# Optimization experiments

Measured on AMD Instinct MI355X. Metric: run time of the kernel, lower is better.

The kernel has to match this reference:

```python
import jax, jax.numpy as jnp
import numpy as np

N = 50000      # nodes
E = 800000     # edges
F = 32         # num_features (per-irrep channels, L=1 -> scalar + vector parts)
NINV = 128     # num_inv_features
NL = 4         # num_layers
H = 64         # edge-MLP hidden width (mlp_params)
G = 2048       # number of graphs
EPS = 1e-6


def setup_inputs() -> dict:
    key = jax.random.key(0)
    ks = jax.random.split(key, 24)
    inp = {
        "x": jax.random.normal(ks[0], (N, 5), jnp.float32),
        "pos": jax.random.normal(ks[1], (N, 3), jnp.float32),
        "edge_index": jax.random.randint(ks[2], (2, E), 0, N, jnp.int64),
        "edge_attr": jax.random.uniform(ks[3], (E, 4), jnp.float32),
        "batch": jnp.sort(jax.random.randint(ks[4], (N,), 0, G, jnp.int64)),
        # embedding block params (scalar and vector branches)
        "W_es": jax.random.normal(ks[5], (5, F), jnp.float32) * 0.3,
        "b_es": jnp.zeros((F,), jnp.float32),
        "W_ev": jax.random.normal(ks[6], (5, F), jnp.float32) * 0.3,
        # per-layer message-passing params, stacked over layers
        "W1": jax.random.normal(ks[7], (NL, 5, H), jnp.float32) * 0.3,
        "b1": jnp.zeros((NL, H), jnp.float32),
        "W2": jax.random.normal(ks[8], (NL, H, 3 * F), jnp.float32) * 0.1,
        "b2": jnp.zeros((NL, 3 * F), jnp.float32),
        "Ws": jax.random.normal(ks[9], (NL, F, F), jnp.float32) * 0.1,
        "Wv": jax.random.normal(ks[10], (NL, F, F), jnp.float32) * 0.1,
        # invariant map
        "W_inv": jax.random.normal(ks[11], (2 * F, NINV), jnp.float32) * 0.1,
        "b_inv": jnp.zeros((NINV,), jnp.float32),
        # fc head: BN -> ELU -> Linear -> BN -> ELU -> Linear(->1)
        "g1": jnp.ones((NINV,), jnp.float32),
        "be1": jnp.zeros((NINV,), jnp.float32),
        "Wf1": jax.random.normal(ks[12], (NINV, NINV), jnp.float32) * 0.1,
        "bf1": jnp.zeros((NINV,), jnp.float32),
        "g2": jnp.ones((NINV,), jnp.float32),
        "be2": jnp.zeros((NINV,), jnp.float32),
        "Wf2": jax.random.normal(ks[13], (NINV, 1), jnp.float32) * 0.1,
        "bf2": jnp.zeros((1,), jnp.float32),
    }
    return inp


def _bn(z, g, b):
    m = z.mean(0)
    va = z.var(0)
    return (z - m) * jax.lax.rsqrt(va + 1e-5) * g + b


def reference(x, pos, edge_index, edge_attr, batch,
              W_es, b_es, W_ev, W1, b1, W2, b2, Ws, Wv,
              W_inv, b_inv, g1, be1, Wf1, bf1, g2, be2, Wf2, bf2):
    src, dst = edge_index[0], edge_index[1]
    delta = pos[dst] - pos[src]                       # [E,3]
    d = jnp.sqrt(jnp.sum(delta * delta, -1) + EPS)    # [E]
    u = delta / d[:, None]                            # unit edge direction

    # embedding: L=1 steerable features = scalar [N,F] + vector [N,F,3]
    s = x @ W_es + b_es
    v = (x @ W_ev)[:, :, None] * pos[:, None, :]

    edge_in = jnp.concatenate([d[:, None], edge_attr], -1)   # [E,5]
    counts = jax.ops.segment_sum(jnp.ones((E,), s.dtype), dst, num_segments=N)
    denom = jnp.maximum(counts, 1.0)[:, None]

    for l in range(NL):  # residual message-passing blocks
        h = jax.nn.elu(edge_in @ W1[l] + b1[l]) @ W2[l] + b2[l]  # [E,3F]
        gs, gv, gsv = jnp.split(h, 3, axis=-1)
        ms = gs * s[src]                                          # [E,F]
        mv = gv[:, :, None] * v[src] + (gsv * s[src])[:, :, None] * u[:, None, :]  # [E,F,3]
        as_ = jax.ops.segment_sum(ms, dst, num_segments=N) / denom
        av = jax.ops.segment_sum(mv, dst, num_segments=N) / denom[:, :, None]
        s = s + jax.nn.elu(as_ @ Ws[l])
        v = v + jnp.einsum('nfd,fg->ngd', av, Wv[l])

    # invariant map: scalars + vector norms
    inv_feats = jnp.concatenate([s, jnp.sqrt(jnp.sum(v * v, -1) + EPS)], -1)
    inv = inv_feats @ W_inv + b_inv                               # [N,NINV]

    # global mean pool over graphs
    gcnt = jnp.maximum(jax.ops.segment_sum(jnp.ones((N,), inv.dtype), batch, num_segments=G), 1.0)[:, None]
    xg = jax.ops.segment_sum(inv, batch, num_segments=G) / gcnt   # [G,NINV]

    z = jax.nn.elu(_bn(xg, g1, be1)) @ Wf1 + bf1
    z = jax.nn.elu(_bn(z, g2, be2)) @ Wf2 + bf2                   # [G,1]
    return z
```

## Files before the change

### kernel.cpp

```cpp
#include <hip/hip_runtime.h>
#include <hip/hip_bf16.h>
#include <math.h>

#define NN 50000
#define EE 800000
#define FF 32
#define HH 64
#define GG 2048
#define NLAYERS 4
#define EPSF 1e-6f
#define TILES 4
#define SCAN_BLOCKS ((NN + 255) / 256)

typedef __attribute__((ext_vector_type(8))) short short8;
typedef __attribute__((ext_vector_type(4))) float f32x4;
typedef __attribute__((ext_vector_type(4))) unsigned short us4;

__device__ __forceinline__ float elu_f(float x){ return x > 0.0f ? x : __expf(x) - 1.0f; }
__device__ __forceinline__ short f2bf_s(float x){
    __hip_bfloat16 h = __float2bfloat16(x);
    return *reinterpret_cast<short*>(&h);
}
__device__ __forceinline__ float bf2f(unsigned short u){
    unsigned int w = ((unsigned int)u) << 16;
    return *reinterpret_cast<float*>(&w);
}

__global__ __launch_bounds__(256) void k_count(const int* __restrict__ ei, int* __restrict__ counts)
{
    int e = blockIdx.x*256 + threadIdx.x;
    if (e >= EE) return;
    atomicAdd(&counts[ei[EE+e]], 1);
}

__global__ __launch_bounds__(256) void k_bsum(const int* __restrict__ counts, int* __restrict__ bsum)
{
    int i = blockIdx.x*256 + threadIdx.x;
    int v = (i < NN) ? counts[i] : 0;
    #pragma unroll
    for (int o=32; o>0; o>>=1) v += __shfl_down(v, o, 64);
    __shared__ int ws[4];
    if ((threadIdx.x & 63) == 0) ws[threadIdx.x >> 6] = v;
    __syncthreads();
    if (threadIdx.x == 0) bsum[blockIdx.x] = ws[0]+ws[1]+ws[2]+ws[3];
}

__global__ __launch_bounds__(256) void k_bscan(const int* __restrict__ bsum, int* __restrict__ boff,
                                               int* __restrict__ rowptr_last)
{
    int t = threadIdx.x;
    int v = (t < SCAN_BLOCKS) ? bsum[t] : 0;
    __shared__ int sh[256];
    sh[t] = v; __syncthreads();
    for (int o=1; o<256; o<<=1){
        int u = (t >= o) ? sh[t-o] : 0;
        __syncthreads();
        sh[t] += u;
        __syncthreads();
    }
    if (t < SCAN_BLOCKS) boff[t] = sh[t] - v;
    if (t == 255) rowptr_last[0] = sh[255];
}

__global__ __launch_bounds__(256) void k_rowptr(const int* __restrict__ counts,
                                                const int* __restrict__ boff, int* __restrict__ rowptr)
{
    int i = blockIdx.x*256 + threadIdx.x;
    int t = threadIdx.x;
    int v = (i < NN) ? counts[i] : 0;
    __shared__ int sh[256];
    sh[t] = v; __syncthreads();
    for (int o=1; o<256; o<<=1){
        int u = (t >= o) ? sh[t-o] : 0;
        __syncthreads();
        sh[t] += u;
        __syncthreads();
    }
    if (i < NN) rowptr[i] = boff[blockIdx.x] + sh[t] - v;
}

__global__ __launch_bounds__(256) void k_fill(
    const int* __restrict__ ei, const float* __restrict__ pos, const float* __restrict__ eattr,
    const int* __restrict__ rowptr, int* __restrict__ cursor,
    int* __restrict__ esrc, float* __restrict__ ein8)
{
    int e = blockIdx.x*256 + threadIdx.x;
    if (e >= EE) return;
    int src = ei[e], dst = ei[EE+e];
    float dx = pos[dst*3+0]-pos[src*3+0];
    float dy = pos[dst*3+1]-pos[src*3+1];
    float dz = pos[dst*3+2]-pos[src*3+2];
    float d = sqrtf(dx*dx+dy*dy+dz*dz+EPSF);
    float inv = 1.0f/d;
    int slot = rowptr[dst] + atomicAdd(&cursor[dst], 1);
    esrc[slot] = src;
    float4* p = (float4*)(ein8 + (size_t)slot*8);
    p[0] = make_float4(d, eattr[e*4+0], eattr[e*4+1], eattr[e*4+2]);
    p[1] = make_float4(eattr[e*4+3], dx*inv, dy*inv, dz*inv);
}

__global__ __launch_bounds__(256) void k_embed(
    const float* __restrict__ x, const float* __restrict__ pos,
    const float* __restrict__ W_es, const float* __restrict__ b_es,
    const float* __restrict__ W_ev,
    float* __restrict__ ns, float* __restrict__ nv, __hip_bfloat16* __restrict__ nbf)
{
    int tid = blockIdx.x*256 + threadIdx.x;
    if (tid >= NN*FF) return;
    int n = tid >> 5, f = tid & 31;
    float x0=x[n*5+0], x1=x[n*5+1], x2=x[n*5+2], x3=x[n*5+3], x4=x[n*5+4];
    float s  = b_es[f] + x0*W_es[f] + x1*W_es[32+f] + x2*W_es[64+f] + x3*W_es[96+f] + x4*W_es[128+f];
    float vm =           x0*W_ev[f] + x1*W_ev[32+f] + x2*W_ev[64+f] + x3*W_ev[96+f] + x4*W_ev[128+f];
    float v0 = vm*pos[n*3+0], v1 = vm*pos[n*3+1], v2 = vm*pos[n*3+2];
    ns[tid] = s;
    nv[n*96+f*3+0] = v0;
    nv[n*96+f*3+1] = v1;
    nv[n*96+f*3+2] = v2;
    us4 q;
    q[0] = (unsigned short)f2bf_s(s);
    q[1] = (unsigned short)f2bf_s(v0);
    q[2] = (unsigned short)f2bf_s(v1);
    q[3] = (unsigned short)f2bf_s(v2);
    *(us4*)((unsigned short*)nbf + (size_t)n*128 + f*4) = q;
}

__global__ __launch_bounds__(256) void k_transpose(
    const float* __restrict__ W2, __hip_bfloat16* __restrict__ W2bf,
    const float* __restrict__ W_inv, __hip_bfloat16* __restrict__ WinvT)
{
    int tid = blockIdx.x*256 + threadIdx.x;
    if (tid < NLAYERS*6144){
        int l = tid / 6144; int r = tid - l*6144;
        int j = r >> 6; int k = r & 63;
        W2bf[l*6144 + j*64 + k] = __float2bfloat16(W2[l*6144 + k*96 + j]);
    } else if (tid < NLAYERS*6144 + 8192){
        int r = tid - NLAYERS*6144;
        int n = r >> 6, k = r & 63;
        WinvT[n*64 + k] = __float2bfloat16(W_inv[k*128 + n]);
    }
}

__global__ __launch_bounds__(256) void k_mlp_mfma(
    const float* __restrict__ ein8,
    const float* __restrict__ W1l, const float* __restrict__ b1l,
    const __hip_bfloat16* __restrict__ W2bfl, const float* __restrict__ b2l,
    __hip_bfloat16* __restrict__ hbuf)
{
    __shared__ __align__(16) __hip_bfloat16 cstage[2][64][104];
    const int tid  = threadIdx.x;
    const int lane = tid & 63;
    const int wave = tid >> 6;
    const int m    = lane & 15;
    const int quad = lane >> 4;

    for (int t=0; t<TILES; t++){
        const long long blockbase = ((long long)blockIdx.x*TILES + t) * 64;
        const long long edge = blockbase + wave*16 + m;

        const float4* p = (const float4*)(ein8 + edge*8);
        float4 q0 = p[0], q1 = p[1];
        float e0=q0.x, e1=q0.y, e2=q0.z, e3=q0.w, e4=q1.x;

        short8 afrag[2];
        #pragma unroll
        for (int s=0;s<2;s++){
            #pragma unroll
            for (int j=0;j<8;j++){
                int k = s*32 + quad*8 + j;
                float a = b1l[k] + e0*W1l[k] + e1*W1l[64+k] + e2*W1l[128+k]
                                 + e3*W1l[192+k] + e4*W1l[256+k];
                afrag[s][j] = f2bf_s(elu_f(a));
            }
        }

        f32x4 acc[6];
        #pragma unroll
        for (int u=0;u<6;u++) acc[u] = (f32x4){0.f,0.f,0.f,0.f};

        #pragma unroll
        for (int s=0;s<2;s++){
            #pragma unroll
            for (int u=0;u<6;u++){
                int n = u*16 + m;
                short8 bfrag = *(const short8*)(W2bfl + n*64 + s*32 + quad*8);
                acc[u] = __builtin_amdgcn_mfma_f32_16x16x32_bf16(afrag[s], bfrag, acc[u], 0, 0, 0);
            }
        }

        __hip_bfloat16 (*cs)[104] = cstage[t&1];
        #pragma unroll
        for (int u=0;u<6;u++){
            int n = u*16 + m;
            float bias = b2l[n];
            #pragma unroll
            for (int r=0;r<4;r++){
                cs[wave*16 + quad*4 + r][n] = __float2bfloat16(acc[u][r] + bias);
            }
        }
        __syncthreads();

        #pragma unroll
        for (int it=0; it<3; it++){
            int flat = it*256 + tid;
            int e = flat / 12, seg = flat % 12;
            float4 val = *(const float4*)&cs[e][seg*8];
            *(float4*)(hbuf + (blockbase + e)*96 + seg*8) = val;
        }
    }
}

__global__ __launch_bounds__(256) void k_agg(
    const int* __restrict__ rowptr, const int* __restrict__ esrc,
    const float* __restrict__ ein8, const __hip_bfloat16* __restrict__ hbuf,
    float* __restrict__ ns, float* __restrict__ nv,
    const __hip_bfloat16* __restrict__ nbfi,
    const float* __restrict__ Wsl, const float* __restrict__ Wvl,
    __hip_bfloat16* __restrict__ nbfo)
{
    int tid = blockIdx.x*256 + threadIdx.x;
    int n = tid >> 5, f = tid & 31;
    if (n >= NN) return;
    int beg = rowptr[n], end = rowptr[n+1];
    float as=0.f, a0=0.f, a1=0.f, a2=0.f;
    if (beg < end){
        const unsigned short* hb = (const unsigned short*)hbuf;
        const unsigned short* nb = (const unsigned short*)nbfi;
        const int last = end - 1;
        int srcs[4];
        #pragma unroll
        for (int j=0;j<4;j++) srcs[j] = esrc[min(beg+j, last)];
        for (int sb=beg; sb<end; sb+=4){
            int srcsN[4];
            #pragma unroll
            for (int j=0;j<4;j++) srcsN[j] = esrc[min(sb+4+j, last)];
            float4 u[4]; unsigned short hx[4],hy[4],hz[4]; us4 nq[4];
            #pragma unroll
            for (int j=0;j<4;j++){
                int sl = min(sb+j, last);
                u[j] = *(const float4*)(ein8 + (size_t)sl*8 + 4);
                size_t ho = (size_t)sl*96;
                hx[j]=hb[ho+f]; hy[j]=hb[ho+32+f]; hz[j]=hb[ho+64+f];
                nq[j] = *(const us4*)(nb + (size_t)srcs[j]*128 + f*4);
            }
            #pragma unroll
            for (int j=0;j<4;j++){
                if (sb+j < end){
                    float gs = bf2f(hx[j]), gv = bf2f(hy[j]), gsv = bf2f(hz[j]);
                    float s  = bf2f(nq[j][0]);
                    float v0 = bf2f(nq[j][1]), v1 = bf2f(nq[j][2]), v2 = bf2f(nq[j][3]);
                    float c = gsv*s;
                    as += gs*s;
                    a0 += gv*v0 + c*u[j].y;
                    a1 += gv*v1 + c*u[j].z;
                    a2 += gv*v2 + c*u[j].w;
                }
            }
            #pragma unroll
            for (int j=0;j<4;j++) srcs[j] = srcsN[j];
        }
    }
    float invd = 1.f/fmaxf((float)(end-beg), 1.f);
    as*=invd; a0*=invd; a1*=invd; a2*=invd;
    float os=0.f, o0=0.f, o1=0.f, o2=0.f;
    #pragma unroll
    for (int k=0;k<FF;k++){
        float bs = __shfl(as, k, 32);
        float b0 = __shfl(a0, k, 32);
        float b1 = __shfl(a1, k, 32);
        float b2 = __shfl(a2, k, 32);
        float ws = Wsl[k*32+f];
        float wv = Wvl[k*32+f];
        os += bs*ws; o0 += b0*wv; o1 += b1*wv; o2 += b2*wv;
    }
    float sn = ns[n*32+f] + elu_f(os);
    float w0 = nv[n*96+f*3+0] + o0;
    float w1 = nv[n*96+f*3+1] + o1;
    float w2 = nv[n*96+f*3+2] + o2;
    ns[n*32+f] = sn;
    nv[n*96+f*3+0] = w0;
    nv[n*96+f*3+1] = w1;
    nv[n*96+f*3+2] = w2;
    us4 q;
    q[0] = (unsigned short)f2bf_s(sn);
    q[1] = (unsigned short)f2bf_s(w0);
    q[2] = (unsigned short)f2bf_s(w1);
    q[3] = (unsigned short)f2bf_s(w2);
    *(us4*)((unsigned short*)nbfo + (size_t)n*128 + f*4) = q;
}

__global__ __launch_bounds__(256) void k_invgemm(
    const float* __restrict__ ns, const float* __restrict__ nv,
    const __hip_bfloat16* __restrict__ WinvT,
    float* __restrict__ inv)
{
    const int tid  = threadIdx.x;
    const int lane = tid & 63;
    const int wave = tid >> 6;
    const int m    = lane & 15;
    const int quad = lane >> 4;
    const int tilebase = blockIdx.x*64 + wave*16;
    const int node = tilebase + m;
    const bool valid = node < NN;

    short8 afrag[2];
    #pragma unroll
    for (int j=0;j<8;j++){
        int k = quad*8 + j;
        float fs = valid ? ns[(size_t)node*32 + k] : 0.f;
        afrag[0][j] = f2bf_s(fs);
        float v0 = valid ? nv[(size_t)node*96 + k*3+0] : 0.f;
        float v1 = valid ? nv[(size_t)node*96 + k*3+1] : 0.f;
        float v2 = valid ? nv[(size_t)node*96 + k*3+2] : 0.f;
        afrag[1][j] = f2bf_s(sqrtf(v0*v0+v1*v1+v2*v2+EPSF));
    }
    f32x4 acc[8];
    #pragma unroll
    for (int t=0;t<8;t++) acc[t] = (f32x4){0.f,0.f,0.f,0.f};
    #pragma unroll
    for (int s=0;s<2;s++){
        #pragma unroll
        for (int t=0;t<8;t++){
            short8 bfrag = *(const short8*)(WinvT + (t*16+m)*64 + s*32 + quad*8);
            acc[t] = __builtin_amdgcn_mfma_f32_16x16x32_bf16(afrag[s], bfrag, acc[t], 0, 0, 0);
        }
    }
    #pragma unroll
    for (int r=0;r<4;r++){
        int nrow = tilebase + quad*4 + r;
        if (nrow < NN){
            #pragma unroll
            for (int t=0;t<8;t++){
                inv[(size_t)nrow*128 + t*16 + m] = acc[t][r];
            }
        }
    }
}

__global__ __launch_bounds__(128) void k_pool(
    const int* __restrict__ batch, const float* __restrict__ inv,
    const float* __restrict__ b_inv, float* __restrict__ xg)
{
    int g = blockIdx.x, j = threadIdx.x;
    int lo = 0, hi = NN;
    while (lo < hi){ int mid=(lo+hi)>>1; if (batch[mid] < g) lo=mid+1; else hi=mid; }
    int beg = lo;
    lo = 0; hi = NN;
    while (lo < hi){ int mid=(lo+hi)>>1; if (batch[mid] < g+1) lo=mid+1; else hi=mid; }
    int end = lo;
    float acc = 0.f;
    for (int n=beg; n<end; n++) acc += inv[(size_t)n*128 + j];
    int cnt = end - beg;
    float cp = fmaxf((float)cnt, 1.f);
    xg[g*128+j] = acc/cp + b_inv[j]*((float)cnt/cp);
}

__global__ __launch_bounds__(256) void k_colstats(
    const float* __restrict__ in, float* __restrict__ mean, float* __restrict__ rstd)
{
    int j = blockIdx.x;
    float s=0.f, q=0.f;
    for (int g=threadIdx.x; g<GG; g+=256){
        float x = in[g*128+j];
        s += x; q += x*x;
    }
    __shared__ float rs[256], rq[256];
    rs[threadIdx.x]=s; rq[threadIdx.x]=q;
    __syncthreads();
    for (int st=128; st>0; st>>=1){
        if (threadIdx.x < st){ rs[threadIdx.x]+=rs[threadIdx.x+st]; rq[threadIdx.x]+=rq[threadIdx.x+st]; }
        __syncthreads();
    }
    if (threadIdx.x==0){
        float m = rs[0]/(float)GG;
        float v = rq[0]/(float)GG - m*m;
        mean[j]=m; rstd[j]=rsqrtf(v+1e-5f);
    }
}

__global__ __launch_bounds__(128) void k_fc1(
    const float* __restrict__ xg, const float* __restrict__ mean, const float* __restrict__ rstd,
    const float* __restrict__ g1, const float* __restrict__ be1,
    const float* __restrict__ Wf1, const float* __restrict__ bf1,
    float* __restrict__ z1)
{
    int g = blockIdx.x, j = threadIdx.x;
    __shared__ float a[128];
    float xin = xg[g*128+j];
    a[j] = elu_f((xin-mean[j])*rstd[j]*g1[j]+be1[j]);
    __syncthreads();
    float z = bf1[j];
    #pragma unroll 8
    for (int k=0;k<128;k++) z += a[k]*Wf1[k*128+j];
    z1[g*128+j] = z;
}

__global__ __launch_bounds__(128) void k_out(
    const float* __restrict__ z1, const float* __restrict__ mean, const float* __restrict__ rstd,
    const float* __restrict__ g2, const float* __restrict__ be2,
    const float* __restrict__ Wf2, const float* __restrict__ bf2,
    float* __restrict__ out)
{
    int g = blockIdx.x, j = threadIdx.x;
    float a = elu_f((z1[g*128+j]-mean[j])*rstd[j]*g2[j]+be2[j]) * Wf2[j];
    __shared__ float red[128];
    red[j]=a; __syncthreads();
    for (int st=64; st>0; st>>=1){
        if (j<st) red[j]+=red[j+st];
        __syncthreads();
    }
    if (j==0) out[g] = red[0] + bf2[0];
}

extern "C" void kernel_launch(void* const* d_in, const int* in_sizes, int n_in,
                              void* d_out, int out_size, void* d_ws, size_t ws_size,
                              hipStream_t stream)
{
    const float* x      = (const float*)d_in[0];
    const float* pos    = (const float*)d_in[1];
    const int*   ei     = (const int*)d_in[2];
    const float* eattr  = (const float*)d_in[3];
    const int*   batch  = (const int*)d_in[4];
    const float* W_es   = (const float*)d_in[5];
    const float* b_es   = (const float*)d_in[6];
    const float* W_ev   = (const float*)d_in[7];
    const float* W1     = (const float*)d_in[8];
    const float* b1     = (const float*)d_in[9];
    const float* W2     = (const float*)d_in[10];
    const float* b2     = (const float*)d_in[11];
    const float* Ws     = (const float*)d_in[12];
    const float* Wv     = (const float*)d_in[13];
    const float* W_inv  = (const float*)d_in[14];
    const float* b_inv  = (const float*)d_in[15];
    const float* g1     = (const float*)d_in[16];
    const float* be1    = (const float*)d_in[17];
    const float* Wf1    = (const float*)d_in[18];
    const float* bf1    = (const float*)d_in[19];
    const float* g2     = (const float*)d_in[20];
    const float* be2    = (const float*)d_in[21];
    const float* Wf2    = (const float*)d_in[22];
    const float* bf2    = (const float*)d_in[23];
    float* out = (float*)d_out;

    char* base = (char*)d_ws;
    size_t off = 0;
    auto alloc = [&](size_t elems4) {
        void* p = base + off;
        off += ((elems4*4 + 63) & ~size_t(63));
        return p;
    };
    int*   counts = (int*)  alloc(50000);
    int*   cursor = (int*)  alloc(50000);
    size_t zero_bytes = off;
    int*   rowptr = (int*)  alloc(50001);
    int*   bsum   = (int*)  alloc(SCAN_BLOCKS);
    int*   boff   = (int*)  alloc(SCAN_BLOCKS);
    int*   esrc   = (int*)  alloc(800000);
    float* ein8   = (float*)alloc(6400000);
    float* ns     = (float*)alloc(1600000);
    float* nv     = (float*)alloc(4800000);
    __hip_bfloat16* nbfA = (__hip_bfloat16*)alloc(3200000);
    __hip_bfloat16* nbfB = (__hip_bfloat16*)alloc(3200000);
    __hip_bfloat16* W2bf = (__hip_bfloat16*)alloc(12288);
    __hip_bfloat16* WinvT= (__hip_bfloat16*)alloc(4096);
    float* xg     = (float*)alloc(262144);
    float* z1     = (float*)alloc(262144);
    float* m1     = (float*)alloc(128);
    float* r1     = (float*)alloc(128);
    float* m2     = (float*)alloc(128);
    float* r2     = (float*)alloc(128);
    __hip_bfloat16* hbuf = (__hip_bfloat16*)alloc(38400000);
    float* inv    = (float*)hbuf;

    hipMemsetAsync(d_ws, 0, zero_bytes, stream);

    k_count    <<<EE/256, 256, 0, stream>>>(ei, counts);
    k_bsum     <<<SCAN_BLOCKS, 256, 0, stream>>>(counts, bsum);
    k_bscan    <<<1, 256, 0, stream>>>(bsum, boff, rowptr + NN);
    k_rowptr   <<<SCAN_BLOCKS, 256, 0, stream>>>(counts, boff, rowptr);
    k_fill     <<<EE/256, 256, 0, stream>>>(ei, pos, eattr, rowptr, cursor, esrc, ein8);
    k_embed    <<<NN*FF/256, 256, 0, stream>>>(x, pos, W_es, b_es, W_ev, ns, nv, nbfA);
    k_transpose<<<(NLAYERS*6144+8192+255)/256, 256, 0, stream>>>(W2, W2bf, W_inv, WinvT);

    for (int l=0; l<NLAYERS; l++){
        const __hip_bfloat16* nbfi = (l&1) ? nbfB : nbfA;
        __hip_bfloat16* nbfo = (l&1) ? nbfA : nbfB;
        k_mlp_mfma<<<EE/(64*TILES), 256, 0, stream>>>(ein8,
            W1 + l*320, b1 + l*64, W2bf + l*6144, b2 + l*96, hbuf);
        k_agg<<<(NN*32+255)/256, 256, 0, stream>>>(rowptr, esrc, ein8, hbuf,
            ns, nv, nbfi, Ws + l*1024, Wv + l*1024, nbfo);
    }

    k_invgemm <<<(NN+63)/64, 256, 0, stream>>>(ns, nv, WinvT, inv);
    k_pool    <<<GG, 128, 0, stream>>>(batch, inv, b_inv, xg);
    k_colstats<<<128, 256, 0, stream>>>(xg, m1, r1);
    k_fc1     <<<GG, 128, 0, stream>>>(xg, m1, r1, g1, be1, Wf1, bf1, z1);
    k_colstats<<<128, 256, 0, stream>>>(z1, m2, r2);
    k_out     <<<GG, 128, 0, stream>>>(z1, m2, r2, g2, be2, Wf2, bf2, out);
}
```

Baseline: 808.5 us.

## Fuse edge MLP into per-node aggregation kernel, drop global hbuf

Merges the edge-MLP MFMA kernel and the aggregation kernel into one per-layer kernel. Each block takes 8 consecutive destination nodes, computes the MLP gate outputs for their CSR edge range in chunks of 128 and stages them in shared memory, then aggregates from LDS. This removes the write and re-read of the large bf16 per-edge buffer each layer. In exchange, per-block edge counts vary, there are extra syncthreads per chunk, partially filled tiles waste MFMA work, and there are fewer blocks.

Result: slower. 1.173 ms (+45.0%).

```diff
diff --git a/kernel.cpp b/kernel.cpp
--- a/kernel.cpp
+++ b/kernel.cpp
@@ -9,8 +9,9 @@
 #define GG 2048
 #define NLAYERS 4
 #define EPSF 1e-6f
-#define TILES 4
 #define SCAN_BLOCKS ((NN + 255) / 256)
+#define NPB 8
+#define CHUNK 128
 
 typedef __attribute__((ext_vector_type(8))) short short8;
 typedef __attribute__((ext_vector_type(4))) float f32x4;
@@ -140,126 +141,124 @@
     }
 }
 
-__global__ __launch_bounds__(256) void k_mlp_mfma(
+__global__ __launch_bounds__(256) void k_layer(
+    const int* __restrict__ rowptr, const int* __restrict__ esrc,
     const float* __restrict__ ein8,
     const float* __restrict__ W1l, const float* __restrict__ b1l,
     const __hip_bfloat16* __restrict__ W2bfl, const float* __restrict__ b2l,
-    __hip_bfloat16* __restrict__ hbuf)
-{
-    __shared__ __align__(16) __hip_bfloat16 cstage[2][64][104];
+    float* __restrict__ ns, float* __restrict__ nv,
+    const __hip_bfloat16* __restrict__ nbfi,
+    const float* __restrict__ Wsl, const float* __restrict__ Wvl,
+    __hip_bfloat16* __restrict__ nbfo)
+{
+    __shared__ __align__(16) __hip_bfloat16 hs[CHUNK][104];
+    __shared__ float us_[CHUNK][4];
     const int tid  = threadIdx.x;
     const int lane = tid & 63;
     const int wave = tid >> 6;
     const int m    = lane & 15;
     const int quad = lane >> 4;
 
-    for (int t=0; t<TILES; t++){
-        const long long blockbase = ((long long)blockIdx.x*TILES + t) * 64;
-        const long long edge = blockbase + wave*16 + m;
-
-        const float4* p = (const float4*)(ein8 + edge*8);
-        float4 q0 = p[0], q1 = p[1];
-        float e0=q0.x, e1=q0.y, e2=q0.z, e3=q0.w, e4=q1.x;
-
-        short8 afrag[2];
+    const int n0 = blockIdx.x * NPB;
+    const int blkbeg = rowptr[n0];
+    const int blkend = rowptr[n0 + NPB];
+
+    const int nloc = tid >> 5;
+    const int f    = tid & 31;
+    const int n    = n0 + nloc;
+    const int nbeg = rowptr[n], nend = rowptr[n+1];
+
+    float as=0.f, a0=0.f, a1=0.f, a2=0.f;
+    const unsigned short* nb = (const unsigned short*)nbfi;
+
+    for (int cbeg = blkbeg; cbeg < blkend; cbeg += CHUNK){
+        const int cend = min(cbeg + CHUNK, blkend);
         #pragma unroll
-        for (int s=0;s<2;s++){
-            #pragma unroll
-            for (int j=0;j<8;j++){
-                int k = s*32 + quad*8 + j;
-                float a = b1l[k] + e0*W1l[k] + e1*W1l[64+k] + e2*W1l[128+k]
-                                 + e3*W1l[192+k] + e4*W1l[256+k];
-                afrag[s][j] = f2bf_s(elu_f(a));
+        for (int t2=0; t2<2; t2++){
+            int tilebase = cbeg + wave*32 + t2*16;
+            if (tilebase < cend){
+                long long edge = (long long)min(tilebase + m, EE-1);
+                const float4* p = (const float4*)(ein8 + edge*8);
+                float4 q0 = p[0], q1 = p[1];
+                if (quad == 0 && tilebase + m < cend){
+                    int si = tilebase + m - cbeg;
+                    us_[si][0]=q1.y; us_[si][1]=q1.z; us_[si][2]=q1.w;
+                }
+                float e0=q0.x, e1=q0.y, e2=q0.z, e3=q0.w, e4=q1.x;
+                short8 afrag[2];
+                #pragma unroll
+                for (int s=0;s<2;s++){
+                    #pragma unroll
+                    for (int j=0;j<8;j++){
+                        int k = s*32 + quad*8 + j;
+                        float a = b1l[k] + e0*W1l[k] + e1*W1l[64+k] + e2*W1l[128+k]
+                                         + e3*W1l[192+k] + e4*W1l[256+k];
+                        afrag[s][j] = f2bf_s(elu_f(a));
+                    }
+                }
+                f32x4 acc[6];
+                #pragma unroll
+                for (int u=0;u<6;u++) acc[u] = (f32x4){0.f,0.f,0.f,0.f};
+                #pragma unroll
+                for (int s=0;s<2;s++){
+                    #pragma unroll
+                    for (int u=0;u<6;u++){
+                        int nn_ = u*16 + m;
+                        short8 bfrag = *(const short8*)(W2bfl + nn_*64 + s*32 + quad*8);
+                        acc[u] = __builtin_amdgcn_mfma_f32_16x16x32_bf16(afrag[s], bfrag, acc[u], 0, 0, 0);
+                    }
+                }
+                int srow = tilebase - cbeg;
+                #pragma unroll
+                for (int u=0;u<6;u++){
+                    int nn_ = u*16 + m;
+                    float bias = b2l[nn_];
+                    #pragma unroll
+                    for (int r=0;r<4;r++){
+                        hs[srow + quad*4 + r][nn_] = __float2bfloat16(acc[u][r] + bias);
+                    }
+                }
             }
         }
-
-        f32x4 acc[6];
-        #pragma unroll
-        for (int u=0;u<6;u++) acc[u] = (f32x4){0.f,0.f,0.f,0.f};
-
-        #pragma unroll
-        for (int s=0;s<2;s++){
+        __syncthreads();
+        int s0 = max(nbeg, cbeg), s1 = min(nend, cend);
+        if (s0 < s1){
+            const int last = s1 - 1;
+            int srcs[4];
             #pragma unroll
-            for (int u=0;u<6;u++){
-                int n = u*16 + m;
-                short8 bfrag = *(const short8*)(W2bfl + n*64 + s*32 + quad*8);
-                acc[u] = __builtin_amdgcn_mfma_f32_16x16x32_bf16(afrag[s], bfrag, acc[u], 0, 0, 0);
+            for (int j=0;j<4;j++) srcs[j] = esrc[min(s0+j, last)];
+            for (int sb=s0; sb<s1; sb+=4){
+                int srcsN[4];
+                #pragma unroll
+                for (int j=0;j<4;j++) srcsN[j] = esrc[min(sb+4+j, last)];
+                us4 nq[4];
+                #pragma unroll
+                for (int j=0;j<4;j++) nq[j] = *(const us4*)(nb + (size_t)srcs[j]*128 + f*4);
+                #pragma unroll
+                for (int j=0;j<4;j++){
+                    int sl = sb + j;
+                    if (sl < s1){
+                        int si = sl - cbeg;
+                        float gs  = bf2f((unsigned short)*(const short*)&hs[si][f]);
+                        float gv  = bf2f((unsigned short)*(const short*)&hs[si][32+f]);
+                        float gsv = bf2f((unsigned short)*(const short*)&hs[si][64+f]);
+                        float s   = bf2f(nq[j][0]);
+                        float v0  = bf2f(nq[j][1]), v1 = bf2f(nq[j][2]), v2 = bf2f(nq[j][3]);
+                        float c = gsv*s;
+                        as += gs*s;
+                        a0 += gv*v0 + c*us_[si][0];
+                        a1 += gv*v1 + c*us_[si][1];
+                        a2 += gv*v2 + c*us_[si][2];
+                    }
+                }
+                #pragma unroll
+                for (int j=0;j<4;j++) srcs[j] = srcsN[j];
             }
         }
-
-        __hip_bfloat16 (*cs)[104] = cstage[t&1];
-        #pragma unroll
-        for (int u=0;u<6;u++){
-            int n = u*16 + m;
-            float bias = b2l[n];
-            #pragma unroll
-            for (int r=0;r<4;r++){
-                cs[wave*16 + quad*4 + r][n] = __float2bfloat16(acc[u][r] + bias);
-            }
-        }
-        __syncthreads();
-
-        #pragma unroll
-        for (int it=0; it<3; it++){
-            int flat = it*256 + tid;
-            int e = flat / 12, seg = flat % 12;
-            float4 val = *(const float4*)&cs[e][seg*8];
-            *(float4*)(hbuf + (blockbase + e)*96 + seg*8) = val;
-        }
-    }
-}
-
-__global__ __launch_bounds__(256) void k_agg(
-    const int* __restrict__ rowptr, const int* __restrict__ esrc,
-    const float* __restrict__ ein8, const __hip_bfloat16* __restrict__ hbuf,
-    float* __restrict__ ns, float* __restrict__ nv,
-    const __hip_bfloat16* __restrict__ nbfi,
-    const float* __restrict__ Wsl, const float* __restrict__ Wvl,
-    __hip_bfloat16* __restrict__ nbfo)
-{
-    int tid = blockIdx.x*256 + threadIdx.x;
-    int n = tid >> 5, f = tid & 31;
-    if (n >= NN) return;
-    int beg = rowptr[n], end = rowptr[n+1];
-    float as=0.f, a0=0.f, a1=0.f, a2=0.f;
-    if (beg < end){
-        const unsigned short* hb = (const unsigned short*)hbuf;
-        const unsigned short* nb = (const unsigned short*)nbfi;
-        const int last = end - 1;
-        int srcs[4];
-        #pragma unroll
-        for (int j=0;j<4;j++) srcs[j] = esrc[min(beg+j, last)];
-        for (int sb=beg; sb<end; sb+=4){
-            int srcsN[4];
-            #pragma unroll
-            for (int j=0;j<4;j++) srcsN[j] = esrc[min(sb+4+j, last)];
-            float4 u[4]; unsigned short hx[4],hy[4],hz[4]; us4 nq[4];
-            #pragma unroll
-            for (int j=0;j<4;j++){
-                int sl = min(sb+j, last);
-                u[j] = *(const float4*)(ein8 + (size_t)sl*8 + 4);
-                size_t ho = (size_t)sl*96;
-                hx[j]=hb[ho+f]; hy[j]=hb[ho+32+f]; hz[j]=hb[ho+64+f];
-                nq[j] = *(const us4*)(nb + (size_t)srcs[j]*128 + f*4);
-            }
-            #pragma unroll
-            for (int j=0;j<4;j++){
-                if (sb+j < end){
-                    float gs = bf2f(hx[j]), gv = bf2f(hy[j]), gsv = bf2f(hz[j]);
-                    float s  = bf2f(nq[j][0]);
-                    float v0 = bf2f(nq[j][1]), v1 = bf2f(nq[j][2]), v2 = bf2f(nq[j][3]);
-                    float c = gsv*s;
-                    as += gs*s;
-                    a0 += gv*v0 + c*u[j].y;
-                    a1 += gv*v1 + c*u[j].z;
-                    a2 += gv*v2 + c*u[j].w;
-                }
-            }
-            #pragma unroll
-            for (int j=0;j<4;j++) srcs[j] = srcsN[j];
-        }
-    }
-    float invd = 1.f/fmaxf((float)(end-beg), 1.f);
+        __syncthreads();
+    }
+
+    float invd = 1.f/fmaxf((float)(nend-nbeg), 1.f);
     as*=invd; a0*=invd; a1*=invd; a2*=invd;
     float os=0.f, o0=0.f, o1=0.f, o2=0.f;
     #pragma unroll
@@ -468,8 +467,7 @@
     float* r1     = (float*)alloc(128);
     float* m2     = (float*)alloc(128);
     float* r2     = (float*)alloc(128);
-    __hip_bfloat16* hbuf = (__hip_bfloat16*)alloc(38400000);
-    float* inv    = (float*)hbuf;
+    float* inv    = (float*)alloc(6400000);
 
     hipMemsetAsync(d_ws, 0, zero_bytes, stream);
 
@@ -484,9 +482,8 @@
     for (int l=0; l<NLAYERS; l++){
         const __hip_bfloat16* nbfi = (l&1) ? nbfB : nbfA;
         __hip_bfloat16* nbfo = (l&1) ? nbfA : nbfB;
-        k_mlp_mfma<<<EE/(64*TILES), 256, 0, stream>>>(ein8,
-            W1 + l*320, b1 + l*64, W2bf + l*6144, b2 + l*96, hbuf);
-        k_agg<<<(NN*32+255)/256, 256, 0, stream>>>(rowptr, esrc, ein8, hbuf,
+        k_layer<<<NN/NPB, 256, 0, stream>>>(rowptr, esrc, ein8,
+            W1 + l*320, b1 + l*64, W2bf + l*6144, b2 + l*96,
             ns, nv, nbfi, Ws + l*1024, Wv + l*1024, nbfo);
     }
 
```
